# Performance work log

Measured on AMD Instinct MI355X. Metric: run time of the kernel, lower is better.

Reference implementation:

```python
import jax, jax.numpy as jnp
import numpy as np

DIM = 1024
N_HEADS = 16
N_KV = 4
HEAD_DIM = DIM // N_HEADS          # 64
GROUP = N_HEADS // N_KV            # 4
KV_DIM = N_KV * HEAD_DIM           # 256
B, S = 2, 2048


def setup_inputs() -> dict:
    key = jax.random.key(0)
    ks = jax.random.split(key, 5)
    scale = 1.0 / np.sqrt(DIM)
    return {
        "x": jax.random.normal(ks[0], (B, S, DIM), dtype=jnp.float32),
        "W_qkv": jax.random.normal(ks[1], (DIM, DIM + 2 * KV_DIM), dtype=jnp.float32) * scale,
        "b_qkv": jnp.zeros((DIM + 2 * KV_DIM,), dtype=jnp.float32),
        "W_out": jax.random.normal(ks[2], (DIM, DIM), dtype=jnp.float32) * scale,
        "b_out": jnp.zeros((DIM,), dtype=jnp.float32),
    }


def reference(x, W_qkv, b_qkv, W_out, b_out):
    b, s, d = x.shape
    qkv = x @ W_qkv + b_qkv                                   # [b, s, dim + 2*kv_dim]
    q, k, v = jnp.split(qkv, [DIM, DIM + KV_DIM], axis=-1)
    # q: [b, n_kv, group, s, hd]; k, v: [b, n_kv, s, hd]
    q = q.reshape(b, s, N_HEADS, HEAD_DIM).transpose(0, 2, 1, 3)
    q = q.reshape(b, N_KV, GROUP, s, HEAD_DIM)
    k = k.reshape(b, s, N_KV, HEAD_DIM).transpose(0, 2, 1, 3)
    v = v.reshape(b, s, N_KV, HEAD_DIM).transpose(0, 2, 1, 3)
    scores = jnp.einsum("bkgsd,bktd->bkgst", q, k) / np.sqrt(HEAD_DIM)
    causal = jnp.tril(jnp.ones((s, s), dtype=bool))           # [s, s]
    scores = jnp.where(causal, scores, -jnp.inf)
    attn = jax.nn.softmax(scores, axis=-1)                    # dropout = 0 (eval)
    y = jnp.einsum("bkgst,bktd->bkgsd", attn, v)              # [b, n_kv, g, s, hd]
    y = y.reshape(b, N_HEADS, s, HEAD_DIM).transpose(0, 2, 1, 3).reshape(b, s, d)
    return y @ W_out + b_out
```

## Files before the change

### kernel.cpp

```cpp
#include <hip/hip_runtime.h>
#include <cstdint>
#include <cstddef>

typedef __bf16 bf16x8 __attribute__((ext_vector_type(8)));
typedef __bf16 bf16x4 __attribute__((ext_vector_type(4)));
typedef float  f32x4  __attribute__((ext_vector_type(4)));

#define DIMD 1024
#define SEQ  2048
#define NB   2
#define NH   16
#define HD   64
#define QKVN 1536
#define VOFF 1280
#define VSTR 2080
#define CSC  0.18033688011112042f

typedef __attribute__((address_space(1))) const void* as1_cvp;
typedef __attribute__((address_space(3))) void* as3_vp;
#define GLL16(g, l) __builtin_amdgcn_global_load_lds((as1_cvp)(const void*)(g), (as3_vp)(void*)(l), 16, 0, 0)

__global__ void cvt_f32_bf16(const float* __restrict__ in, __bf16* __restrict__ out, int n4) {
    int i = blockIdx.x * blockDim.x + threadIdx.x;
    if (i >= n4) return;
    float4 v = reinterpret_cast<const float4*>(in)[i];
    bf16x4 o;
    o[0] = (__bf16)v.x; o[1] = (__bf16)v.y; o[2] = (__bf16)v.z; o[3] = (__bf16)v.w;
    reinterpret_cast<bf16x4*>(out)[i] = o;
}

__global__ void transpose_cvt(const float* __restrict__ in, __bf16* __restrict__ out, int R, int C) {
    __shared__ float t[32][33];
    int bx = blockIdx.x * 32;
    int by = blockIdx.y * 32;
    int tx = threadIdx.x, ty = threadIdx.y;
#pragma unroll
    for (int i = 0; i < 32; i += 8)
        t[ty + i][tx] = in[(size_t)(by + ty + i) * C + bx + tx];
    __syncthreads();
#pragma unroll
    for (int i = 0; i < 32; i += 8)
        out[(size_t)(bx + ty + i) * R + by + tx] = (__bf16)t[tx][ty + i];
}

__global__ void transpose_v(const __bf16* __restrict__ qkv, __bf16* __restrict__ vtg) {
    __shared__ __bf16 t[32][34];
    const int z = blockIdx.z;
    const int b = z >> 2, kh = z & 3;
    const int s0 = blockIdx.x * 32, d0 = blockIdx.y * 32;
    const int tx = threadIdx.x, ty = threadIdx.y;
    const __bf16* src = qkv + (size_t)b * SEQ * QKVN + VOFF + kh * HD;
#pragma unroll
    for (int i = 0; i < 32; i += 8)
        t[ty + i][tx] = src[(size_t)(s0 + ty + i) * QKVN + d0 + tx];
    __syncthreads();
    __bf16* dst = vtg + ((size_t)z * HD + d0) * VSTR + s0;
#pragma unroll
    for (int i = 0; i < 32; i += 8)
        dst[(size_t)(ty + i) * VSTR + tx] = t[tx][ty + i];
}

template<int OUT_BF16, int QSCALE>
__global__ __launch_bounds__(256) void gemm_bf16(
    const __bf16* __restrict__ A, const __bf16* __restrict__ Bt,
    const float* __restrict__ bias, void* __restrict__ Cout,
    int M, int N, int K)
{
    __shared__ __bf16 Als[128 * 32];
    __shared__ __bf16 Bls[128 * 32];
    const int tid  = threadIdx.x;
    const int lane = tid & 63;
    const int wave = tid >> 6;
    const int lo = lane & 15, hi = lane >> 4;
    const int bm = blockIdx.y * 128, bn = blockIdx.x * 128;
    const int wr = (wave >> 1) * 64, wc = (wave & 1) * 64;

    const __bf16* gA = A  + (size_t)(bm + wave * 32 + (lane >> 2)) * K + (lane & 3) * 8;
    const __bf16* gB = Bt + (size_t)(bn + wave * 32 + (lane >> 2)) * K + (lane & 3) * 8;
    __bf16* lA = &Als[wave * 32 * 32];
    __bf16* lB = &Bls[wave * 32 * 32];

    f32x4 acc[4][4] = {};

    for (int k0 = 0; k0 < K; k0 += 32) {
        __syncthreads();
        GLL16(gA + k0,                  lA);
        GLL16(gA + k0 + (size_t)16 * K, lA + 512);
        GLL16(gB + k0,                  lB);
        GLL16(gB + k0 + (size_t)16 * K, lB + 512);
        __syncthreads();

        bf16x8 af[4], bfr[4];
#pragma unroll
        for (int i = 0; i < 4; i++) {
            af[i]  = *reinterpret_cast<const bf16x8*>(&Als[(wr + i * 16 + lo) * 32 + hi * 8]);
            bfr[i] = *reinterpret_cast<const bf16x8*>(&Bls[(wc + i * 16 + lo) * 32 + hi * 8]);
        }
#pragma unroll
        for (int i = 0; i < 4; i++)
#pragma unroll
            for (int j = 0; j < 4; j++)
                acc[i][j] = __builtin_amdgcn_mfma_f32_16x16x32_bf16(af[i], bfr[j], acc[i][j], 0, 0, 0);
    }

#pragma unroll
    for (int j = 0; j < 4; j++) {
        int col = bn + wc + j * 16 + lo;
        float bv = bias[col];
#pragma unroll
        for (int i = 0; i < 4; i++) {
            int row0 = bm + wr + i * 16 + hi * 4;
#pragma unroll
            for (int rr = 0; rr < 4; rr++) {
                float v = acc[i][j][rr] + bv;
                if (QSCALE && col < DIMD) v *= CSC;
                if (OUT_BF16) ((__bf16*)Cout)[(size_t)(row0 + rr) * N + col] = (__bf16)v;
                else          ((float* )Cout)[(size_t)(row0 + rr) * N + col] = v;
            }
        }
    }
}

__global__ __launch_bounds__(512, 4) void attn_fwd(
    const __bf16* __restrict__ qkv, const __bf16* __restrict__ vt, __bf16* __restrict__ y)
{
    __shared__ __bf16 Kls[128 * 64];
    __shared__ __bf16 Vls[64 * 128];
    __shared__ __bf16 Pls[8][2][16][72];
    const int tid  = threadIdx.x;
    const int wave = tid >> 6, lane = tid & 63;
    const int lo = lane & 15, hi = lane >> 4;
    const int head = wave & 3, par = wave >> 2;

    const int bid = blockIdx.x;
    const int z  = bid & 7;
    const int b  = z >> 2, kh = z & 3;
    const int p  = bid >> 3;
    const int h  = kh * 4 + head;

    const int TA = p, TB = 127 - p;
    const int qwA = TA * 16, qwB = TB * 16;
    const int cA = (TA >> 2) + 1, cB = (TB >> 2) + 1;
    const int nsc = (cB + 1) >> 1;

    const __bf16* base = qkv + (size_t)b * SEQ * QKVN;
    const __bf16* qp = base + h * HD;
    const __bf16* kp = base + DIMD + kh * HD;
    const __bf16* vp = vt + (size_t)z * HD * VSTR;

    const int srow = lane >> 3;
    const int sun  = ((lane & 7) ^ srow) * 8;
    const __bf16* kst0 = kp + (size_t)(wave * 16 + srow) * QKVN + sun;
    const __bf16* kst1 = kp + (size_t)(wave * 16 + 8 + srow) * QKVN + sun;
    const int vrow = lane >> 4;
    const int vun0 = ((lane & 15) ^ vrow) * 8;
    const int vun1 = ((lane & 15) ^ (vrow + 4)) * 8;
    const __bf16* vst0 = vp + (size_t)(wave * 8 + vrow) * VSTR + vun0;
    const __bf16* vst1 = vp + (size_t)(wave * 8 + 4 + vrow) * VSTR + vun1;
    __bf16* kdst = &Kls[wave * 1024];
    __bf16* vdst = &Vls[wave * 1024];

#define STAGE(s)                                            \
    do {                                                    \
        const size_t ko = (size_t)(s) * 128 * QKVN;         \
        const int    vo = (s) * 128;                        \
        GLL16(kst0 + ko, kdst);                             \
        GLL16(kst1 + ko, kdst + 512);                       \
        GLL16(vst0 + vo, vdst);                             \
        GLL16(vst1 + vo, vdst + 512);                       \
    } while (0)

    const int xk = lo & 7;
    const int u0 = (hi ^ xk) * 8;
    const int u1 = ((hi + 4) ^ xk) * 8;
    const int kb = par * 64;

    bf16x8 bQA0 = *reinterpret_cast<const bf16x8*>(qp + (size_t)(qwA + lo) * QKVN + hi * 8);
    bf16x8 bQA1 = *reinterpret_cast<const bf16x8*>(qp + (size_t)(qwA + lo) * QKVN + 32 + hi * 8);
    bf16x8 bQB0 = *reinterpret_cast<const bf16x8*>(qp + (size_t)(qwB + lo) * QKVN + hi * 8);
    bf16x8 bQB1 = *reinterpret_cast<const bf16x8*>(qp + (size_t)(qwB + lo) * QKVN + 32 + hi * 8);

    f32x4 accA[4] = {}, accB[4] = {};
    float ssA = 0.0f, ssB = 0.0f;

    STAGE(0);
    __syncthreads();

    for (int s = 0; s < nsc; ++s) {
        const int ce = 2 * s + par;
        const int kt = ce << 6;
        const bool aB = (ce < cB), dB = (ce == cB - 1);
        const bool aA = (ce < cA), dA = (ce == cA - 1);

        if (aB) {
#pragma unroll
            for (int ks = 0; ks < 4; ks++) {
                const __bf16* Kr = &Kls[(kb + ks * 16 + lo) * 64];
                bf16x8 aK0 = *reinterpret_cast<const bf16x8*>(Kr + u0);
                bf16x8 aK1 = *reinterpret_cast<const bf16x8*>(Kr + u1);

                {
                    f32x4 sv = {0.f, 0.f, 0.f, 0.f};
                    sv = __builtin_amdgcn_mfma_f32_16x16x32_bf16(aK0, bQB0, sv, 0, 0, 0);
                    sv = __builtin_amdgcn_mfma_f32_16x16x32_bf16(aK1, bQB1, sv, 0, 0, 0);
                    bf16x4 pk;
#pragma unroll
                    for (int r = 0; r < 4; r++) {
                        float e = exp2f(sv[r]);
                        if (dB && (kt + ks * 16 + hi * 4 + r > qwB + lo)) e = 0.0f;
                        ssB += e;
                        pk[r] = (__bf16)e;
                    }
                    *reinterpret_cast<bf16x4*>(&Pls[wave][1][lo][ks * 16 + hi * 4]) = pk;
                }
                if (aA) {
                    f32x4 sv = {0.f, 0.f, 0.f, 0.f};
                    sv = __builtin_amdgcn_mfma_f32_16x16x32_bf16(aK0, bQA0, sv, 0, 0, 0);
                    sv = __builtin_amdgcn_mfma_f32_16x16x32_bf16(aK1, bQA1, sv, 0, 0, 0);
                    bf16x4 pk;
#pragma unroll
                    for (int r = 0; r < 4; r++) {
                        float e = exp2f(sv[r]);
                        if (dA && (kt + ks * 16 + hi * 4 + r > qwA + lo)) e = 0.0f;
                        ssA += e;
                        pk[r] = (__bf16)e;
                    }
                    *reinterpret_cast<bf16x4*>(&Pls[wave][0][lo][ks * 16 + hi * 4]) = pk;
                }
            }

#pragma unroll
            for (int k2 = 0; k2 < 2; k2++) {
                const int uv = ((8 * par + k2 * 4 + hi) ^ xk) * 8;
                bf16x8 v0 = *reinterpret_cast<const bf16x8*>(&Vls[(0 * 16 + lo) * 128] + uv);
                bf16x8 v1 = *reinterpret_cast<const bf16x8*>(&Vls[(1 * 16 + lo) * 128] + uv);
                bf16x8 v2 = *reinterpret_cast<const bf16x8*>(&Vls[(2 * 16 + lo) * 128] + uv);
                bf16x8 v3 = *reinterpret_cast<const bf16x8*>(&Vls[(3 * 16 + lo) * 128] + uv);
                bf16x8 pB = *reinterpret_cast<const bf16x8*>(&Pls[wave][1][lo][k2 * 32 + hi * 8]);
                accB[0] = __builtin_amdgcn_mfma_f32_16x16x32_bf16(pB, v0, accB[0], 0, 0, 0);
                accB[1] = __builtin_amdgcn_mfma_f32_16x16x32_bf16(pB, v1, accB[1], 0, 0, 0);
                accB[2] = __builtin_amdgcn_mfma_f32_16x16x32_bf16(pB, v2, accB[2], 0, 0, 0);
                accB[3] = __builtin_amdgcn_mfma_f32_16x16x32_bf16(pB, v3, accB[3], 0, 0, 0);
                if (aA) {
                    bf16x8 pA = *reinterpret_cast<const bf16x8*>(&Pls[wave][0][lo][k2 * 32 + hi * 8]);
                    accA[0] = __builtin_amdgcn_mfma_f32_16x16x32_bf16(pA, v0, accA[0], 0, 0, 0);
                    accA[1] = __builtin_amdgcn_mfma_f32_16x16x32_bf16(pA, v1, accA[1], 0, 0, 0);
                    accA[2] = __builtin_amdgcn_mfma_f32_16x16x32_bf16(pA, v2, accA[2], 0, 0, 0);
                    accA[3] = __builtin_amdgcn_mfma_f32_16x16x32_bf16(pA, v3, accA[3], 0, 0, 0);
                }
            }
        }

        __syncthreads();
        if (s + 1 < nsc) {
            STAGE(s + 1);
            __syncthreads();
        }
    }
#undef STAGE

    float* cls = (float*)&Pls[0][0][0][0];
    const int cbase = (head * 64 + lane) * 36;
    if (par == 1) {
#pragma unroll
        for (int f = 0; f < 4; f++) {
            *reinterpret_cast<f32x4*>(&cls[cbase + f * 4])      = accA[f];
            *reinterpret_cast<f32x4*>(&cls[cbase + 16 + f * 4]) = accB[f];
        }
        cls[cbase + 32] = ssA;
        cls[cbase + 33] = ssB;
    }
    __syncthreads();
    if (par == 0) {
#pragma unroll
        for (int f = 0; f < 4; f++) {
            accA[f] += *reinterpret_cast<f32x4*>(&cls[cbase + f * 4]);
            accB[f] += *reinterpret_cast<f32x4*>(&cls[cbase + 16 + f * 4]);
        }
        ssA += cls[cbase + 32];
        ssB += cls[cbase + 33];

        ssA += __shfl_xor(ssA, 16);  ssA += __shfl_xor(ssA, 32);
        ssB += __shfl_xor(ssB, 16);  ssB += __shfl_xor(ssB, 32);
#pragma unroll
        for (int r = 0; r < 4; r++) {
            float srA = __shfl(ssA, hi * 4 + r);
            float srB = __shfl(ssB, hi * 4 + r);
            float invA = 1.0f / srA, invB = 1.0f / srB;
            int qA = qwA + hi * 4 + r, qB = qwB + hi * 4 + r;
#pragma unroll
            for (int f = 0; f < 4; f++) {
                y[(size_t)(b * SEQ + qA) * DIMD + h * HD + f * 16 + lo] = (__bf16)(accA[f][r] * invA);
                y[(size_t)(b * SEQ + qB) * DIMD + h * HD + f * 16 + lo] = (__bf16)(accB[f][r] * invB);
            }
        }
    }
}

extern "C" void kernel_launch(void* const* d_in, const int* in_sizes, int n_in,
                              void* d_out, int out_size, void* d_ws, size_t ws_size,
                              hipStream_t stream) {
    const float* x    = (const float*)d_in[0];
    const float* Wqkv = (const float*)d_in[1];
    const float* bqkv = (const float*)d_in[2];
    const float* Wout = (const float*)d_in[3];
    const float* bout = (const float*)d_in[4];
    float* out = (float*)d_out;

    char* ws = (char*)d_ws;
    __bf16* xb    = (__bf16*)(ws);
    __bf16* wqkvT = (__bf16*)(ws + ((size_t)8  << 20));
    __bf16* woutT = (__bf16*)(ws + ((size_t)11 << 20));
    __bf16* qkvb  = (__bf16*)(ws + ((size_t)13 << 20));
    __bf16* vtg   = wqkvT;
    __bf16* yb    = xb;

    const int M = NB * SEQ;

    cvt_f32_bf16<<<(M * DIMD / 4 + 255) / 256, 256, 0, stream>>>(x, xb, M * DIMD / 4);
    transpose_cvt<<<dim3(QKVN / 32, DIMD / 32), dim3(32, 8), 0, stream>>>(Wqkv, wqkvT, DIMD, QKVN);
    transpose_cvt<<<dim3(DIMD / 32, DIMD / 32), dim3(32, 8), 0, stream>>>(Wout, woutT, DIMD, DIMD);

    gemm_bf16<1, 1><<<dim3(QKVN / 128, M / 128), 256, 0, stream>>>(xb, wqkvT, bqkv, qkvb, M, QKVN, DIMD);

    transpose_v<<<dim3(SEQ / 32, HD / 32, NB * 4), dim3(32, 8), 0, stream>>>(qkvb, vtg);

    attn_fwd<<<512, 512, 0, stream>>>(qkvb, vtg, yb);

    gemm_bf16<0, 0><<<dim3(DIMD / 128, M / 128), 256, 0, stream>>>(yb, woutT, bout, out, M, DIMD, DIMD);
}
```

Before: 116.7 us.

## Fuse prep kernels into one launch and retile GEMMs to 128x64 with XCD swizzle

Merges the x conversion and both weight transpose-converts into a single prep kernel, which removes two launches. The GEMMs change from 128x128 to 128x64 tiles, doubling the block count so the device's CUs are better filled. Blocks are remapped with a modulo-8 swizzle so neighbouring tiles land on the same XCD and share L2. Smaller tiles lower the MFMA-to-load ratio and re-read A more often.

```diff
diff --git a/kernel.cpp b/kernel.cpp
--- a/kernel.cpp
+++ b/kernel.cpp
@@ -20,27 +20,42 @@
 typedef __attribute__((address_space(3))) void* as3_vp;
 #define GLL16(g, l) __builtin_amdgcn_global_load_lds((as1_cvp)(const void*)(g), (as3_vp)(void*)(l), 16, 0, 0)
 
-__global__ void cvt_f32_bf16(const float* __restrict__ in, __bf16* __restrict__ out, int n4) {
-    int i = blockIdx.x * blockDim.x + threadIdx.x;
-    if (i >= n4) return;
-    float4 v = reinterpret_cast<const float4*>(in)[i];
-    bf16x4 o;
-    o[0] = (__bf16)v.x; o[1] = (__bf16)v.y; o[2] = (__bf16)v.z; o[3] = (__bf16)v.w;
-    reinterpret_cast<bf16x4*>(out)[i] = o;
-}
-
-__global__ void transpose_cvt(const float* __restrict__ in, __bf16* __restrict__ out, int R, int C) {
+__global__ __launch_bounds__(256) void prep(
+    const float* __restrict__ x, __bf16* __restrict__ xb,
+    const float* __restrict__ Wqkv, __bf16* __restrict__ wqkvT,
+    const float* __restrict__ Wout, __bf16* __restrict__ woutT)
+{
     __shared__ float t[32][33];
-    int bx = blockIdx.x * 32;
-    int by = blockIdx.y * 32;
-    int tx = threadIdx.x, ty = threadIdx.y;
+    const int bidx = blockIdx.x;
+    const int tid  = threadIdx.x;
+
+    if (bidx < 4096) {
+        int i = bidx * 256 + tid;
+        float4 v = reinterpret_cast<const float4*>(x)[i];
+        bf16x4 o;
+        o[0] = (__bf16)v.x; o[1] = (__bf16)v.y; o[2] = (__bf16)v.z; o[3] = (__bf16)v.w;
+        reinterpret_cast<bf16x4*>(xb)[i] = o;
+        return;
+    }
+
+    const float* in; __bf16* out; int C, bx, by;
+    if (bidx < 5632) {
+        int idx = bidx - 4096;
+        in = Wqkv; out = wqkvT; C = QKVN;
+        bx = idx % 48; by = idx / 48;
+    } else {
+        int idx = bidx - 5632;
+        in = Wout; out = woutT; C = DIMD;
+        bx = idx & 31; by = idx >> 5;
+    }
+    const int tx = tid & 31, ty = tid >> 5;
 #pragma unroll
     for (int i = 0; i < 32; i += 8)
-        t[ty + i][tx] = in[(size_t)(by + ty + i) * C + bx + tx];
+        t[ty + i][tx] = in[(size_t)(by * 32 + ty + i) * C + bx * 32 + tx];
     __syncthreads();
 #pragma unroll
     for (int i = 0; i < 32; i += 8)
-        out[(size_t)(bx + ty + i) * R + by + tx] = (__bf16)t[tx][ty + i];
+        out[(size_t)(bx * 32 + ty + i) * DIMD + by * 32 + tx] = (__bf16)t[tx][ty + i];
 }
 
 __global__ void transpose_v(const __bf16* __restrict__ qkv, __bf16* __restrict__ vtg) {
@@ -64,47 +79,51 @@
 __global__ __launch_bounds__(256) void gemm_bf16(
     const __bf16* __restrict__ A, const __bf16* __restrict__ Bt,
     const float* __restrict__ bias, void* __restrict__ Cout,
-    int M, int N, int K)
+    int M, int N, int K, int nx)
 {
     __shared__ __bf16 Als[128 * 32];
-    __shared__ __bf16 Bls[128 * 32];
+    __shared__ __bf16 Bls[64 * 32];
     const int tid  = threadIdx.x;
     const int lane = tid & 63;
     const int wave = tid >> 6;
     const int lo = lane & 15, hi = lane >> 4;
-    const int bm = blockIdx.y * 128, bn = blockIdx.x * 128;
-    const int wr = (wave >> 1) * 64, wc = (wave & 1) * 64;
-
-    const __bf16* gA = A  + (size_t)(bm + wave * 32 + (lane >> 2)) * K + (lane & 3) * 8;
-    const __bf16* gB = Bt + (size_t)(bn + wave * 32 + (lane >> 2)) * K + (lane & 3) * 8;
-    __bf16* lA = &Als[wave * 32 * 32];
-    __bf16* lB = &Bls[wave * 32 * 32];
-
-    f32x4 acc[4][4] = {};
+
+    const int lin = blockIdx.x;
+    const int cpx = gridDim.x >> 3;
+    const int swz = (lin & 7) * cpx + (lin >> 3);
+    const int bm = (swz / nx) * 128, bn = (swz % nx) * 64;
+    const int wr = (wave >> 1) * 64, wc = (wave & 1) * 32;
+
+    const __bf16* gA = A  + (size_t)(bm + wave * 16 + (lane >> 2)) * K + (lane & 3) * 8;
+    const __bf16* gB = Bt + (size_t)(bn + wave * 16 + (lane >> 2)) * K + (lane & 3) * 8;
+    __bf16* lA = &Als[wave * 16 * 32];
+    __bf16* lB = &Bls[wave * 16 * 32];
+
+    f32x4 acc[4][2] = {};
 
     for (int k0 = 0; k0 < K; k0 += 32) {
         __syncthreads();
         GLL16(gA + k0,                  lA);
-        GLL16(gA + k0 + (size_t)16 * K, lA + 512);
+        GLL16(gA + k0 + (size_t)64 * K, lA + 2048);
         GLL16(gB + k0,                  lB);
-        GLL16(gB + k0 + (size_t)16 * K, lB + 512);
         __syncthreads();
 
-        bf16x8 af[4], bfr[4];
-#pragma unroll
-        for (int i = 0; i < 4; i++) {
-            af[i]  = *reinterpret_cast<const bf16x8*>(&Als[(wr + i * 16 + lo) * 32 + hi * 8]);
-            bfr[i] = *reinterpret_cast<const bf16x8*>(&Bls[(wc + i * 16 + lo) * 32 + hi * 8]);
-        }
+        bf16x8 af[4], bfr[2];
 #pragma unroll
         for (int i = 0; i < 4; i++)
-#pragma unroll
-            for (int j = 0; j < 4; j++)
+            af[i] = *reinterpret_cast<const bf16x8*>(&Als[(wr + i * 16 + lo) * 32 + hi * 8]);
+#pragma unroll
+        for (int j = 0; j < 2; j++)
+            bfr[j] = *reinterpret_cast<const bf16x8*>(&Bls[(wc + j * 16 + lo) * 32 + hi * 8]);
+#pragma unroll
+        for (int i = 0; i < 4; i++)
+#pragma unroll
+            for (int j = 0; j < 2; j++)
                 acc[i][j] = __builtin_amdgcn_mfma_f32_16x16x32_bf16(af[i], bfr[j], acc[i][j], 0, 0, 0);
     }
 
 #pragma unroll
-    for (int j = 0; j < 4; j++) {
+    for (int j = 0; j < 2; j++) {
         int col = bn + wc + j * 16 + lo;
         float bv = bias[col];
 #pragma unroll
@@ -317,15 +336,15 @@
 
     const int M = NB * SEQ;
 
-    cvt_f32_bf16<<<(M * DIMD / 4 + 255) / 256, 256, 0, stream>>>(x, xb, M * DIMD / 4);
-    transpose_cvt<<<dim3(QKVN / 32, DIMD / 32), dim3(32, 8), 0, stream>>>(Wqkv, wqkvT, DIMD, QKVN);
-    transpose_cvt<<<dim3(DIMD / 32, DIMD / 32), dim3(32, 8), 0, stream>>>(Wout, woutT, DIMD, DIMD);
-
-    gemm_bf16<1, 1><<<dim3(QKVN / 128, M / 128), 256, 0, stream>>>(xb, wqkvT, bqkv, qkvb, M, QKVN, DIMD);
+    prep<<<6656, 256, 0, stream>>>(x, xb, Wqkv, wqkvT, Wout, woutT);
+
+    gemm_bf16<1, 1><<<(M / 128) * (QKVN / 64), 256, 0, stream>>>(
+        xb, wqkvT, bqkv, qkvb, M, QKVN, DIMD, QKVN / 64);
 
     transpose_v<<<dim3(SEQ / 32, HD / 32, NB * 4), dim3(32, 8), 0, stream>>>(qkvb, vtg);
 
     attn_fwd<<<512, 512, 0, stream>>>(qkvb, vtg, yb);
 
-    gemm_bf16<0, 0><<<dim3(DIMD / 128, M / 128), 256, 0, stream>>>(yb, woutT, bout, out, M, DIMD, DIMD);
-}
+    gemm_bf16<0, 0><<<(M / 128) * (DIMD / 64), 256, 0, stream>>>(
+        yb, woutT, bout, out, M, DIMD, DIMD, DIMD / 64);
+}
```

After: 104.0 us. 10.9% less time.
